# Kernel tuning notes

Measured on AMD Instinct MI355X. Metric: run time of the kernel, lower is better.

Reference implementation:

```python
import jax, jax.numpy as jnp
import numpy as np

N_ATOMS = 65536
N_BONDS = 262144
MAX_NB = 6
H = 256
ATOM_F = 133
BOND_F = 147
N_MOLS = 2048
STEPS = 3  # message_steps; loop runs STEPS-1 times as in the torch code


def setup_inputs() -> dict:
    key = jax.random.key(0)
    ks = jax.random.split(key, 10)
    f_atoms = jax.random.normal(ks[0], (N_ATOMS, ATOM_F), jnp.float32)
    f_bonds = jax.random.normal(ks[1], (N_BONDS, BOND_F), jnp.float32)
    a2b = jax.random.randint(ks[2], (N_ATOMS, MAX_NB), 0, N_BONDS)
    b2a = jax.random.randint(ks[3], (N_BONDS,), 0, N_ATOMS)
    b2revb = jax.random.randint(ks[4], (N_BONDS,), 0, N_BONDS)
    mol_index = jnp.sort(jax.random.randint(ks[5], (N_ATOMS,), 0, N_MOLS))
    W_i = jax.random.normal(ks[6], (BOND_F, H), jnp.float32) / np.sqrt(BOND_F).astype(np.float32)
    W_m = jax.random.normal(ks[7], (H, H), jnp.float32) / np.sqrt(H).astype(np.float32)
    W_a = jax.random.normal(ks[8], (ATOM_F + H, H), jnp.float32) / np.sqrt(ATOM_F + H).astype(np.float32)
    b_a = jnp.zeros((H,), jnp.float32)
    return {"f_atoms": f_atoms, "f_bonds": f_bonds, "W_i": W_i, "W_m": W_m,
            "W_a": W_a, "b_a": b_a, "a2b": a2b, "b2a": b2a, "b2revb": b2revb,
            "mol_index": mol_index}


def reference(f_atoms, f_bonds, W_i, W_m, W_a, b_a, a2b, b2a, b2revb, mol_index):
    # W_i: bond features -> hidden (no bias), then ReLU
    inp = f_bonds @ W_i                       # [n_bonds, H]
    message = jax.nn.relu(inp)
    # D-MPNN bond-message passing (dropout p=0 / eval mode)
    for _ in range(STEPS - 1):
        agg = message[a2b].sum(axis=1)        # gather [n_atoms, MAX_NB, H] -> sum
        m = agg[b2a] - message[b2revb]        # subtract reverse-bond message
        message = jax.nn.relu(inp + m @ W_m)
    # atom-level aggregation + W_a linear + ReLU
    a_message = message[a2b].sum(axis=1)      # [n_atoms, H]
    a_input = jnp.concatenate([f_atoms, a_message], axis=1)
    atom_h = jax.nn.relu(a_input @ W_a + b_a)
    # ragged per-molecule mean readout via segment ops
    sums = jax.ops.segment_sum(atom_h, mol_index, num_segments=N_MOLS)
    counts = jax.ops.segment_sum(jnp.ones((N_ATOMS,), atom_h.dtype), mol_index,
                                 num_segments=N_MOLS)
    mol_vecs = sums / jnp.maximum(counts, 1.0)[:, None]  # empty mol -> zero vector
    return mol_vecs
```

## Files before the change

### kernel.cpp

```cpp
#include <hip/hip_runtime.h>
#include <cstdint>

#define NA 65536
#define NB 262144
#define MAXNB 6
#define H 256
#define BF 147
#define AF 133
#define NM 2048

typedef unsigned int u32;
typedef __attribute__((ext_vector_type(8))) short bf16x8;
typedef __attribute__((ext_vector_type(4))) float f32x4;

__device__ __forceinline__ u32 pack_bf2(float a, float b) {
    u32 ua = __float_as_uint(a); ua = (ua + 0x7FFFu + ((ua >> 16) & 1u)) >> 16;
    u32 ub = __float_as_uint(b); ub = (ub + 0x7FFFu + ((ub >> 16) & 1u)) >> 16;
    return ua | (ub << 16);
}
__device__ __forceinline__ unsigned short bf1(float a) {
    u32 ua = __float_as_uint(a); return (unsigned short)((ua + 0x7FFFu + ((ua >> 16) & 1u)) >> 16);
}
__device__ __forceinline__ float bf_lo(u32 u) { return __uint_as_float(u << 16); }
__device__ __forceinline__ float bf_hi(u32 u) { return __uint_as_float(u & 0xFFFF0000u); }

__device__ __forceinline__ int tswz(int row, int col) {
    int chunk = (col >> 3) ^ (((row >> 2) & 3) << 1);
    return row * 512 + (chunk << 4) + ((col & 7) << 1);
}

__global__ __launch_bounds__(256) void k_pack_w(const float* __restrict__ W,
                                                uint4* __restrict__ Wp, int K) {
    int t = blockIdx.x * 256 + threadIdx.x;
    int kbg = t >> 8, col = t & 255;
    int k0 = kbg * 8;
    float x[8];
#pragma unroll
    for (int j = 0; j < 8; ++j)
        x[j] = (k0 + j < K) ? W[(size_t)(k0 + j) * 256 + col] : 0.f;
    uint4 o;
    o.x = pack_bf2(x[0], x[1]); o.y = pack_bf2(x[2], x[3]);
    o.z = pack_bf2(x[4], x[5]); o.w = pack_bf2(x[6], x[7]);
    Wp[t] = o;
}

__global__ __launch_bounds__(256) void k_pack_wa(const float* __restrict__ W,
                                                 uint4* __restrict__ Wp) {
    int t = blockIdx.x * 256 + threadIdx.x;
    int kbg = t >> 8, col = t & 255;
    int k0 = kbg * 8;
    float x[8];
#pragma unroll
    for (int j = 0; j < 8; ++j) {
        int c = k0 + j;
        float v = 0.f;
        if (c < AF) v = W[(size_t)c * 256 + col];
        else if (c >= 136 && c < 392) v = W[(size_t)(c - 3) * 256 + col];
        x[j] = v;
    }
    uint4 o;
    o.x = pack_bf2(x[0], x[1]); o.y = pack_bf2(x[2], x[3]);
    o.z = pack_bf2(x[4], x[5]); o.w = pack_bf2(x[6], x[7]);
    Wp[t] = o;
}

__global__ __launch_bounds__(256, 8) void k_gemm_wi(const float* __restrict__ X,
                                                    const uint4* __restrict__ Wp,
                                                    u32* __restrict__ outb) {
    __shared__ char xs[32 * 512];
    const int blk = blockIdx.x;
    const int tid = threadIdx.x;
    const int lane = tid & 63, wv = tid >> 6;
    const int rlo = lane & 15, g = lane >> 4;

    for (int r = wv; r < 32; r += 4) {
        const float* row = X + ((size_t)blk * 32 + r) * BF;
#pragma unroll
        for (int p = 0; p < 2; ++p) {
            int c = p * 128 + lane * 2;
            if (c < 160) {
                float v0 = (c < BF) ? row[c] : 0.f;
                float v1 = (c + 1 < BF) ? row[c + 1] : 0.f;
                *(u32*)(xs + r * 336 + c * 2) = pack_bf2(v0, v1);
            }
        }
    }
    __syncthreads();

    f32x4 acc[2][4] = {};
#pragma unroll
    for (int kb = 0; kb < 5; ++kb) {
        bf16x8 af[2], bfr[4];
#pragma unroll
        for (int rb = 0; rb < 2; ++rb) {
            int row = rb * 16 + rlo;
            af[rb] = *(const bf16x8*)(xs + row * 336 + (kb * 4 + g) * 16);
        }
#pragma unroll
        for (int cb = 0; cb < 4; ++cb) {
            uint4 w = Wp[(size_t)(kb * 4 + g) * 256 + wv * 64 + cb * 16 + rlo];
            bfr[cb] = *(const bf16x8*)&w;
        }
#pragma unroll
        for (int rb = 0; rb < 2; ++rb)
#pragma unroll
            for (int cb = 0; cb < 4; ++cb)
                acc[rb][cb] = __builtin_amdgcn_mfma_f32_16x16x32_bf16(
                    af[rb], bfr[cb], acc[rb][cb], 0, 0, 0);
    }
    __syncthreads();
#pragma unroll
    for (int rb = 0; rb < 2; ++rb)
#pragma unroll
        for (int cb = 0; cb < 4; ++cb)
#pragma unroll
            for (int r = 0; r < 4; ++r)
                *(unsigned short*)(xs + tswz(rb * 16 + g * 4 + r, wv * 64 + cb * 16 + rlo)) =
                    bf1(acc[rb][cb][r]);
    __syncthreads();
#pragma unroll
    for (int i = 0; i < 4; ++i) {
        int e = (i * 256 + tid) * 8;
        int row = e >> 8, col = e & 255;
        uint4 dv = *(const uint4*)(xs + tswz(row, col));
        *(uint4*)&outb[(((size_t)blk * 32 + row) * 256 + col) >> 1] = dv;
    }
}

template <bool RELU_SRC>
__global__ __launch_bounds__(256) void k_agg(const u32* __restrict__ msgb,
                                             const int* __restrict__ a2b,
                                             u32* __restrict__ aggb) {
    const int tid = threadIdx.x;
    const int lane = tid & 63, wv = tid >> 6;
    const int a = blockIdx.x * 4 + wv;
    float4 s = {0.f, 0.f, 0.f, 0.f};
#pragma unroll
    for (int j = 0; j < MAXNB; ++j) {
        int b = a2b[a * MAXNB + j];
        uint2 mv = *(const uint2*)&msgb[(size_t)b * 128 + lane * 2];
        float e0 = bf_lo(mv.x), e1 = bf_hi(mv.x), e2 = bf_lo(mv.y), e3 = bf_hi(mv.y);
        if (RELU_SRC) {
            e0 = fmaxf(e0, 0.f); e1 = fmaxf(e1, 0.f);
            e2 = fmaxf(e2, 0.f); e3 = fmaxf(e3, 0.f);
        }
        s.x += e0; s.y += e1; s.z += e2; s.w += e3;
    }
    uint2 o;
    o.x = pack_bf2(s.x, s.y); o.y = pack_bf2(s.z, s.w);
    *(uint2*)&aggb[(size_t)a * 128 + lane * 2] = o;
}

template <bool RELU_SRC>
__global__ __launch_bounds__(256) void k_msg_update(
    const u32* __restrict__ inpb, const u32* __restrict__ aggb,
    const u32* __restrict__ msgb_in, const int* __restrict__ b2a,
    const int* __restrict__ b2revb, const uint4* __restrict__ Wp,
    u32* __restrict__ msgb_out) {
    __shared__ char xs[64 * 512];
    const int blk = blockIdx.x;
    const int tid = threadIdx.x;
    const int lane = tid & 63, wv = tid >> 6;
    const int rlo = lane & 15, g = lane >> 4;

    int ia = 0, irv = 0;
    if (lane < 16) {
        int b = blk * 64 + wv + lane * 4;
        ia  = b2a[b];
        irv = b2revb[b];
    }
#pragma unroll
    for (int i = 0; i < 16; ++i) {
        const int r = wv + i * 4;
        const int a   = __builtin_amdgcn_readlane(ia, i);
        const int rb_ = __builtin_amdgcn_readlane(irv, i);
        uint2 gv = *(const uint2*)&aggb[(size_t)a * 128 + lane * 2];
        uint2 mv = *(const uint2*)&msgb_in[(size_t)rb_ * 128 + lane * 2];
        float m0 = bf_lo(mv.x), m1 = bf_hi(mv.x), m2 = bf_lo(mv.y), m3 = bf_hi(mv.y);
        if (RELU_SRC) {
            m0 = fmaxf(m0, 0.f); m1 = fmaxf(m1, 0.f);
            m2 = fmaxf(m2, 0.f); m3 = fmaxf(m3, 0.f);
        }
        uint2 pk;
        pk.x = pack_bf2(bf_lo(gv.x) - m0, bf_hi(gv.x) - m1);
        pk.y = pack_bf2(bf_lo(gv.y) - m2, bf_hi(gv.y) - m3);
        int schunk = (lane >> 1) ^ (r & 7);
        *(uint2*)(xs + r * 512 + (schunk << 4) + (lane & 1) * 8) = pk;
    }
    __syncthreads();

    f32x4 acc[4][4] = {};
#pragma unroll
    for (int kb = 0; kb < 8; ++kb) {
        bf16x8 af[4], bfr[4];
#pragma unroll
        for (int rb = 0; rb < 4; ++rb) {
            int row = rb * 16 + rlo;
            int schunk = (kb * 4 + g) ^ (row & 7);
            af[rb] = *(const bf16x8*)(xs + row * 512 + (schunk << 4));
        }
#pragma unroll
        for (int cb = 0; cb < 4; ++cb) {
            uint4 w = Wp[(size_t)(kb * 4 + g) * 256 + wv * 64 + cb * 16 + rlo];
            bfr[cb] = *(const bf16x8*)&w;
        }
#pragma unroll
        for (int rb = 0; rb < 4; ++rb)
#pragma unroll
            for (int cb = 0; cb < 4; ++cb)
                acc[rb][cb] = __builtin_amdgcn_mfma_f32_16x16x32_bf16(
                    af[rb], bfr[cb], acc[rb][cb], 0, 0, 0);
    }
    __syncthreads();

#pragma unroll
    for (int rb = 0; rb < 4; ++rb)
#pragma unroll
        for (int cb = 0; cb < 4; ++cb)
#pragma unroll
            for (int r = 0; r < 4; ++r)
                ((unsigned short*)xs)[(rb * 16 + g * 4 + r) * 256 + wv * 64 + cb * 16 + rlo] =
                    bf1(acc[rb][cb][r]);
    __syncthreads();

#pragma unroll
    for (int i = 0; i < 8; ++i) {
        int e = (i * 256 + tid) * 8;
        int row = e >> 8, col = e & 255;
        uint4 dv = *(const uint4*)(xs + row * 512 + col * 2);
        size_t go = ((size_t)blk * 64 + row) * 256 + col;
        uint4 iv = *(const uint4*)&inpb[go >> 1];
        uint4 ov;
        ov.x = pack_bf2(fmaxf(bf_lo(dv.x) + bf_lo(iv.x), 0.f),
                        fmaxf(bf_hi(dv.x) + bf_hi(iv.x), 0.f));
        ov.y = pack_bf2(fmaxf(bf_lo(dv.y) + bf_lo(iv.y), 0.f),
                        fmaxf(bf_hi(dv.y) + bf_hi(iv.y), 0.f));
        ov.z = pack_bf2(fmaxf(bf_lo(dv.z) + bf_lo(iv.z), 0.f),
                        fmaxf(bf_hi(dv.z) + bf_hi(iv.z), 0.f));
        ov.w = pack_bf2(fmaxf(bf_lo(dv.w) + bf_lo(iv.w), 0.f),
                        fmaxf(bf_hi(dv.w) + bf_hi(iv.w), 0.f));
        *(uint4*)&msgb_out[go >> 1] = ov;
    }
}

__global__ __launch_bounds__(256) void k_atomh(
    const float* __restrict__ f_atoms, const u32* __restrict__ msgb,
    const int* __restrict__ a2b, const uint4* __restrict__ Wp,
    const float* __restrict__ ba, u32* __restrict__ athb) {
    __shared__ char xs[64 * 832];
    const int blk = blockIdx.x;
    const int tid = threadIdx.x;
    const int lane = tid & 63, wv = tid >> 6;
    const int rlo = lane & 15, g = lane >> 4;

    for (int r = wv; r < 64; r += 4) {
        const int gr = blk * 64 + r;
        const float* fa = f_atoms + (size_t)gr * AF;
#pragma unroll
        for (int p = 0; p < 2; ++p) {
            int c = p * 128 + lane * 2;
            if (c < 136) {
                float v0 = (c < AF) ? fa[c] : 0.f;
                float v1 = (c + 1 < AF) ? fa[c + 1] : 0.f;
                *(u32*)(xs + r * 832 + c * 2) = pack_bf2(v0, v1);
            }
        }
        float s0 = 0.f, s1 = 0.f, s2 = 0.f, s3 = 0.f;
#pragma unroll
        for (int j = 0; j < MAXNB; ++j) {
            int b = a2b[gr * MAXNB + j];
            uint2 mv = *(const uint2*)&msgb[(size_t)b * 128 + lane * 2];
            s0 += bf_lo(mv.x); s1 += bf_hi(mv.x);
            s2 += bf_lo(mv.y); s3 += bf_hi(mv.y);
        }
        uint2 o; o.x = pack_bf2(s0, s1); o.y = pack_bf2(s2, s3);
        *(uint2*)(xs + r * 832 + 272 + lane * 8) = o;
        if (lane < 6) {
            uint2 z = {0u, 0u};
            *(uint2*)(xs + r * 832 + 784 + lane * 8) = z;
        }
    }
    __syncthreads();

    f32x4 acc[4][4] = {};
#pragma unroll
    for (int kb = 0; kb < 13; ++kb) {
        bf16x8 af[4], bfr[4];
#pragma unroll
        for (int rb = 0; rb < 4; ++rb) {
            int row = rb * 16 + rlo;
            af[rb] = *(const bf16x8*)(xs + row * 832 + (kb * 4 + g) * 16);
        }
#pragma unroll
        for (int cb = 0; cb < 4; ++cb) {
            uint4 w = Wp[(size_t)(kb * 4 + g) * 256 + wv * 64 + cb * 16 + rlo];
            bfr[cb] = *(const bf16x8*)&w;
        }
#pragma unroll
        for (int rb = 0; rb < 4; ++rb)
#pragma unroll
            for (int cb = 0; cb < 4; ++cb)
                acc[rb][cb] = __builtin_amdgcn_mfma_f32_16x16x32_bf16(
                    af[rb], bfr[cb], acc[rb][cb], 0, 0, 0);
    }
    __syncthreads();
    float bcol[4];
#pragma unroll
    for (int cb = 0; cb < 4; ++cb) bcol[cb] = ba[wv * 64 + cb * 16 + rlo];
#pragma unroll
    for (int rb = 0; rb < 4; ++rb)
#pragma unroll
        for (int cb = 0; cb < 4; ++cb)
#pragma unroll
            for (int r = 0; r < 4; ++r)
                ((unsigned short*)xs)[(rb * 16 + g * 4 + r) * 256 + wv * 64 + cb * 16 + rlo] =
                    bf1(fmaxf(acc[rb][cb][r] + bcol[cb], 0.f));
    __syncthreads();
#pragma unroll
    for (int i = 0; i < 8; ++i) {
        int e = (i * 256 + tid) * 8;
        int row = e >> 8, col = e & 255;
        uint4 dv = *(const uint4*)(xs + row * 512 + col * 2);
        *(uint4*)&athb[(((size_t)blk * 64 + row) * 256 + col) >> 1] = dv;
    }
}

__global__ __launch_bounds__(256) void k_readout(const unsigned short* __restrict__ athb,
                                                 const int* __restrict__ mol_index,
                                                 float* __restrict__ out) {
    __shared__ int s_lo, s_hi;
    const int m = blockIdx.x;
    const int tid = threadIdx.x;
    if (tid == 0) {
        int lo = 0, hi = NA;
        while (lo < hi) { int mid = (lo + hi) >> 1; if (mol_index[mid] < m) lo = mid + 1; else hi = mid; }
        s_lo = lo;
        int lo2 = lo, hi2 = NA;
        while (lo2 < hi2) { int mid = (lo2 + hi2) >> 1; if (mol_index[mid] < m + 1) lo2 = mid + 1; else hi2 = mid; }
        s_hi = lo2;
    }
    __syncthreads();
    const int lo = s_lo, hi = s_hi;
    float s = 0.f;
    for (int a = lo; a < hi; ++a) {
        u32 u = athb[(size_t)a * 256 + tid];
        s += __uint_as_float(u << 16);
    }
    float cnt = (float)(hi - lo);
    out[(size_t)m * 256 + tid] = s / fmaxf(cnt, 1.0f);
}

extern "C" void kernel_launch(void* const* d_in, const int* in_sizes, int n_in,
                              void* d_out, int out_size, void* d_ws, size_t ws_size,
                              hipStream_t stream) {
    const float* f_atoms = (const float*)d_in[0];
    const float* f_bonds = (const float*)d_in[1];
    const float* W_i     = (const float*)d_in[2];
    const float* W_m     = (const float*)d_in[3];
    const float* W_a     = (const float*)d_in[4];
    const float* b_a     = (const float*)d_in[5];
    const int* a2b       = (const int*)d_in[6];
    const int* b2a       = (const int*)d_in[7];
    const int* b2revb    = (const int*)d_in[8];
    const int* mol_index = (const int*)d_in[9];
    float* out = (float*)d_out;

    const size_t SZ_BH2 = (size_t)NB * H * 2;
    const size_t SZ_AG2 = (size_t)NA * H * 2;
    const size_t SZ_WPM = 32 * 256 * 16;
    const size_t SZ_WPI = 20 * 256 * 16;
    const size_t SZ_WPA = 52 * 256 * 16;
    const size_t NEEDED = 3 * SZ_BH2 + SZ_AG2 + SZ_WPM + SZ_WPI + SZ_WPA;
    if (ws_size < NEEDED) return;

    char* ws = (char*)d_ws;
    u32* inp    = (u32*)(ws);
    u32* msg1   = (u32*)(ws + SZ_BH2);
    u32* msg2   = (u32*)(ws + 2 * SZ_BH2);
    u32* aggb   = (u32*)(ws + 3 * SZ_BH2);
    uint4* WpM  = (uint4*)(ws + 3 * SZ_BH2 + SZ_AG2);
    uint4* WpI  = (uint4*)(ws + 3 * SZ_BH2 + SZ_AG2 + SZ_WPM);
    uint4* WpA  = (uint4*)(ws + 3 * SZ_BH2 + SZ_AG2 + SZ_WPM + SZ_WPI);
    u32* athb   = msg1;

    k_pack_w<<<32, 256, 0, stream>>>(W_m, WpM, 256);
    k_pack_w<<<20, 256, 0, stream>>>(W_i, WpI, BF);
    k_pack_wa<<<52, 256, 0, stream>>>(W_a, WpA);

    k_gemm_wi<<<NB / 32, 256, 0, stream>>>(f_bonds, WpI, inp);

    k_agg<true><<<NA / 4, 256, 0, stream>>>(inp, a2b, aggb);
    k_msg_update<true><<<NB / 64, 256, 0, stream>>>(inp, aggb, inp, b2a, b2revb, WpM, msg1);

    k_agg<false><<<NA / 4, 256, 0, stream>>>(msg1, a2b, aggb);
    k_msg_update<false><<<NB / 64, 256, 0, stream>>>(inp, aggb, msg1, b2a, b2revb, WpM, msg2);

    k_atomh<<<NA / 64, 256, 0, stream>>>(f_atoms, msg2, a2b, WpA, b_a, athb);

    k_readout<<<NM, 256, 0, stream>>>((const unsigned short*)athb, mol_index, out);
}
```

Baseline: 484.4 us.

## Split message gather into two halves to overlap second gather with first-half MFMA

The bond-message update kernel now gathers the first 32 rows (agg minus reverse message) into shared memory, syncs, then issues the gathers for the remaining 32 rows before running MFMAs on the first half. A second sync precedes the MFMA pass over the second half. The intent is to hide gather latency behind matrix work. In exchange, W_m fragments are loaded twice from global memory and there is an extra barrier.

New measurement: 524.1 us. 8.2% more time.

```diff
diff --git a/kernel.cpp b/kernel.cpp
--- a/kernel.cpp
+++ b/kernel.cpp
@@ -169,8 +169,9 @@
         ia  = b2a[b];
         irv = b2revb[b];
     }
-#pragma unroll
-    for (int i = 0; i < 16; ++i) {
+
+#pragma unroll
+    for (int i = 0; i < 8; ++i) {
         const int r = wv + i * 4;
         const int a   = __builtin_amdgcn_readlane(ia, i);
         const int rb_ = __builtin_amdgcn_readlane(irv, i);
@@ -189,12 +190,31 @@
     }
     __syncthreads();
 
+#pragma unroll
+    for (int i = 8; i < 16; ++i) {
+        const int r = wv + i * 4;
+        const int a   = __builtin_amdgcn_readlane(ia, i);
+        const int rb_ = __builtin_amdgcn_readlane(irv, i);
+        uint2 gv = *(const uint2*)&aggb[(size_t)a * 128 + lane * 2];
+        uint2 mv = *(const uint2*)&msgb_in[(size_t)rb_ * 128 + lane * 2];
+        float m0 = bf_lo(mv.x), m1 = bf_hi(mv.x), m2 = bf_lo(mv.y), m3 = bf_hi(mv.y);
+        if (RELU_SRC) {
+            m0 = fmaxf(m0, 0.f); m1 = fmaxf(m1, 0.f);
+            m2 = fmaxf(m2, 0.f); m3 = fmaxf(m3, 0.f);
+        }
+        uint2 pk;
+        pk.x = pack_bf2(bf_lo(gv.x) - m0, bf_hi(gv.x) - m1);
+        pk.y = pack_bf2(bf_lo(gv.y) - m2, bf_hi(gv.y) - m3);
+        int schunk = (lane >> 1) ^ (r & 7);
+        *(uint2*)(xs + r * 512 + (schunk << 4) + (lane & 1) * 8) = pk;
+    }
+
     f32x4 acc[4][4] = {};
 #pragma unroll
     for (int kb = 0; kb < 8; ++kb) {
-        bf16x8 af[4], bfr[4];
-#pragma unroll
-        for (int rb = 0; rb < 4; ++rb) {
+        bf16x8 af[2], bfr[4];
+#pragma unroll
+        for (int rb = 0; rb < 2; ++rb) {
             int row = rb * 16 + rlo;
             int schunk = (kb * 4 + g) ^ (row & 7);
             af[rb] = *(const bf16x8*)(xs + row * 512 + (schunk << 4));
@@ -205,11 +225,34 @@
             bfr[cb] = *(const bf16x8*)&w;
         }
 #pragma unroll
-        for (int rb = 0; rb < 4; ++rb)
+        for (int rb = 0; rb < 2; ++rb)
 #pragma unroll
             for (int cb = 0; cb < 4; ++cb)
                 acc[rb][cb] = __builtin_amdgcn_mfma_f32_16x16x32_bf16(
                     af[rb], bfr[cb], acc[rb][cb], 0, 0, 0);
+    }
+    __syncthreads();
+
+#pragma unroll
+    for (int kb = 0; kb < 8; ++kb) {
+        bf16x8 af[2], bfr[4];
+#pragma unroll
+        for (int rb = 2; rb < 4; ++rb) {
+            int row = rb * 16 + rlo;
+            int schunk = (kb * 4 + g) ^ (row & 7);
+            af[rb - 2] = *(const bf16x8*)(xs + row * 512 + (schunk << 4));
+        }
+#pragma unroll
+        for (int cb = 0; cb < 4; ++cb) {
+            uint4 w = Wp[(size_t)(kb * 4 + g) * 256 + wv * 64 + cb * 16 + rlo];
+            bfr[cb] = *(const bf16x8*)&w;
+        }
+#pragma unroll
+        for (int rb = 2; rb < 4; ++rb)
+#pragma unroll
+            for (int cb = 0; cb < 4; ++cb)
+                acc[rb][cb] = __builtin_amdgcn_mfma_f32_16x16x32_bf16(
+                    af[rb - 2], bfr[cb], acc[rb][cb], 0, 0, 0);
     }
     __syncthreads();
 
```
